# Kernel tuning notes

Hardware: AMD Instinct MI355X
Metric: run time of the kernel (lower is better)

Reference implementation:

```python
import jax, jax.numpy as jnp
import numpy as np

NEG_SLOPE = 0.2

def _gat_conv(x, src, dst, W, a_src, a_dst, b, heads, out_ch, concat):
    N = x.shape[0]
    h = (x @ W).reshape(N, heads, out_ch)                      # [N,H,C]
    al_s = jnp.einsum('nhc,hc->nh', h, a_src)                  # [N,H]
    al_d = jnp.einsum('nhc,hc->nh', h, a_dst)
    e = jax.nn.leaky_relu(al_s[src] + al_d[dst], NEG_SLOPE)    # [E,H]
    emax = jax.ops.segment_max(e, dst, num_segments=N)         # [N,H]
    ex = jnp.exp(e - emax[dst])
    denom = jax.ops.segment_sum(ex, dst, num_segments=N)
    alpha = ex / denom[dst]                                    # [E,H]
    msg = h[src] * alpha[:, :, None]                           # [E,H,C]
    out = jax.ops.segment_sum(msg, dst, num_segments=N)        # [N,H,C]
    if concat:
        out = out.reshape(N, heads * out_ch)
    else:
        out = out.mean(axis=1)
    return out + b

def _add_self_loops(edge_index, N):
    loops = jnp.arange(N, dtype=edge_index.dtype)
    src = jnp.concatenate([edge_index[0], loops])
    dst = jnp.concatenate([edge_index[1], loops])
    return src, dst

def setup_inputs() -> dict:
    key = jax.random.key(0)
    ks = jax.random.split(key, 16)
    N, E, Fin, C, H, G, OUT = 50000, 1600000, 128, 32, 8, 256, 64
    s = 0.05
    inp = {
        'x': jax.random.normal(ks[0], (N, Fin), jnp.float32),
        'edge_index': jax.random.randint(ks[1], (2, E), 0, N, jnp.int64),
        'batch': jnp.sort(jax.random.randint(ks[2], (N,), 0, G, jnp.int64)),
        'W0': jax.random.normal(ks[3], (Fin, H * C), jnp.float32) * s,
        'a_src0': jax.random.normal(ks[4], (H, C), jnp.float32) * s,
        'a_dst0': jax.random.normal(ks[5], (H, C), jnp.float32) * s,
        'b0': jnp.zeros((H * C,), jnp.float32),
        'W1': jax.random.normal(ks[6], (H * C, H * C), jnp.float32) * s,
        'a_src1': jax.random.normal(ks[7], (H, C), jnp.float32) * s,
        'a_dst1': jax.random.normal(ks[8], (H, C), jnp.float32) * s,
        'b1': jnp.zeros((H * C,), jnp.float32),
        'W2': jax.random.normal(ks[9], (H * C, C), jnp.float32) * s,
        'a_src2': jax.random.normal(ks[10], (1, C), jnp.float32) * s,
        'a_dst2': jax.random.normal(ks[11], (1, C), jnp.float32) * s,
        'b2': jnp.zeros((C,), jnp.float32),
        'lin_w': jax.random.normal(ks[12], (C, OUT), jnp.float32) * s,
        'lin_b': jnp.zeros((OUT,), jnp.float32),
    }
    return inp

def reference(x, edge_index, batch, W0, a_src0, a_dst0, b0, W1, a_src1, a_dst1, b1,
              W2, a_src2, a_dst2, b2, lin_w, lin_b):
    N = x.shape[0]
    G = 256
    src, dst = _add_self_loops(edge_index, N)
    h = jax.nn.relu(_gat_conv(x, src, dst, W0, a_src0, a_dst0, b0, 8, 32, True))
    h = jax.nn.relu(_gat_conv(h, src, dst, W1, a_src1, a_dst1, b1, 8, 32, True))
    h = _gat_conv(h, src, dst, W2, a_src2, a_dst2, b2, 1, 32, True)  # heads=1 concat -> [N,32]
    # global mean pool over graphs
    sums = jax.ops.segment_sum(h, batch, num_segments=G)
    cnts = jax.ops.segment_sum(jnp.ones((N,), h.dtype), batch, num_segments=G)
    pooled = sums / jnp.maximum(cnts, 1.0)[:, None]
    return pooled @ lin_w + lin_b
```

## Files before the change

### kernel.cpp

```cpp
#include <hip/hip_runtime.h>
#include <hip/hip_bf16.h>


#define LRELU(x) ((x) >= 0.f ? (x) : 0.2f * (x))

typedef unsigned short ushort8 __attribute__((ext_vector_type(8)));
typedef unsigned short ushort4v __attribute__((ext_vector_type(4)));
typedef __attribute__((ext_vector_type(8))) short bf16x8;
typedef __attribute__((ext_vector_type(4))) float f32x4;

__device__ __forceinline__ float bf2f(unsigned short u) {
    return __uint_as_float(((unsigned)u) << 16);
}
__device__ __forceinline__ unsigned short f2bf(float f) {
    __hip_bfloat16 b = __float2bfloat16(f);
    return *reinterpret_cast<unsigned short*>(&b);
}
__device__ __forceinline__ void gl_lds16(const unsigned short* g, unsigned short* l) {
    __builtin_amdgcn_global_load_lds((const __attribute__((address_space(1))) void*)g,
                                     (__attribute__((address_space(3))) void*)l, 16, 0, 0);
}


__global__ void deg_kernel(const int* __restrict__ dst, int* __restrict__ deg,
                           int E, int N) {
    int i = blockIdx.x * blockDim.x + threadIdx.x;
    if (i < E) atomicAdd(&deg[dst[i]], 1);
    else if (i < E + N) atomicAdd(&deg[i - E], 1);
}

__global__ void scan_kernel(const int* __restrict__ deg, int* __restrict__ rowptr, int n,
                            const int* __restrict__ batch, int* __restrict__ gstart,
                            int N, int G) {
    const int tid = threadIdx.x;
    if (tid <= G) {
        int lo = 0, hi = N;
        while (lo < hi) { int mid = (lo + hi) >> 1; if (batch[mid] < tid) lo = mid + 1; else hi = mid; }
        gstart[tid] = lo;
    }
    __shared__ int partial[1024];
    const int chunk = (n + 1023) / 1024;
    const int start = min(tid * chunk, n);
    const int end = min(start + chunk, n);
    int s = 0;
    for (int i = start; i < end; i++) s += deg[i];
    partial[tid] = s;
    __syncthreads();
    for (int o = 1; o < 1024; o <<= 1) {
        int v = (tid >= o) ? partial[tid - o] : 0;
        __syncthreads();
        partial[tid] += v;
        __syncthreads();
    }
    int run = (tid == 0) ? 0 : partial[tid - 1];
    for (int i = start; i < end; i++) { rowptr[i] = run; run += deg[i]; }
    if (tid == 0) rowptr[n] = partial[1023];
}

__global__ void scatter_col_binned(const int* __restrict__ src, const int* __restrict__ dst,
                                   int* __restrict__ rowptr, int* __restrict__ col,
                                   int E, int N, int lo, int hi) {
    int i = blockIdx.x * blockDim.x + threadIdx.x;
    if (i < E) {
        int d = dst[i];
        if (d < lo || d >= hi) return;
        int pos = atomicAdd(&rowptr[d], 1);
        col[pos] = src[i];
    } else if (i < E + N) {
        int d = i - E;
        if (d < lo || d >= hi) return;
        int pos = atomicAdd(&rowptr[d], 1);
        col[pos] = d;
    }
}


__global__ void prep_kernel(const float* __restrict__ x, const float* __restrict__ W0,
                            const float* __restrict__ W1, const float* __restrict__ W2,
                            unsigned short* __restrict__ xb, unsigned short* __restrict__ w0t,
                            unsigned short* __restrict__ w1t, unsigned short* __restrict__ w2t,
                            int N) {
    int i = blockIdx.x * blockDim.x + threadIdx.x;
    int nx = N * 128;
    if (i < nx) { xb[i] = f2bf(x[i]); return; }
    i -= nx;
    if (i < 256 * 128) {
        int n = i / 128, k = i - n * 128;
        w0t[i] = f2bf(W0[(size_t)k * 256 + n]);
        return;
    }
    i -= 256 * 128;
    if (i < 256 * 256) {
        int n = i / 256, k = i - n * 256;
        w1t[i] = f2bf(W1[(size_t)k * 256 + n]);
        return;
    }
    i -= 256 * 256;
    if (i < 32 * 256) {
        int n = i / 256, k = i - n * 256;
        w2t[i] = f2bf(W2[(size_t)k * 32 + n]);
    }
}


template <int BM, int BN, int WM, int WN, int H>
__global__ __launch_bounds__(256)
void gemm_bf16_al(const unsigned short* __restrict__ A, const unsigned short* __restrict__ Bt,
                  unsigned short* __restrict__ Cc,
                  const float* __restrict__ a_src, const float* __restrict__ a_dst,
                  float* __restrict__ als, float* __restrict__ ald,
                  int M, int Nn, int K) {
    constexpr int BK = 64;
    constexpr int MT = WM / 16, NT = WN / 16;
    constexpr int NWX = BN / WN;
    constexpr int NHL = WN / 32;
    __shared__ __attribute__((aligned(16))) unsigned short Ab[BM][BK];
    __shared__ __attribute__((aligned(16))) unsigned short Bb[BN][BK];
    const int tid = threadIdx.x;
    const int lane = tid & 63;
    const int wave = tid >> 6;
    const int wx = wave % NWX, wy = wave / NWX;
    const int by = blockIdx.y * BM;
    const int bx = blockIdx.x * BN;
    const int r16 = lane & 15, kg = lane >> 4;
    const int srow = lane >> 3, sslot = lane & 7;

    f32x4 acc[MT][NT];
#pragma unroll
    for (int i = 0; i < MT; i++)
#pragma unroll
        for (int j = 0; j < NT; j++) acc[i][j] = (f32x4){0.f, 0.f, 0.f, 0.f};

    for (int k0 = 0; k0 < K; k0 += BK) {
        for (int t = wave; t < BM / 8; t += 4) {
            int gm = by + t * 8 + srow;
            if (gm >= M) gm = M - 1;
            gl_lds16(A + (size_t)gm * K + k0 + sslot * 8, &Ab[t * 8][0]);
        }
        for (int t = wave; t < BN / 8; t += 4) {
            int gn = bx + t * 8 + srow;
            gl_lds16(Bt + (size_t)gn * K + k0 + sslot * 8, &Bb[t * 8][0]);
        }
        __syncthreads();
#pragma unroll
        for (int ks = 0; ks < 2; ks++) {
            bf16x8 bh[NT];
#pragma unroll
            for (int j = 0; j < NT; j++)
                bh[j] = *(const bf16x8*)&Bb[wx * WN + j * 16 + r16][ks * 32 + kg * 8];
#pragma unroll
            for (int i = 0; i < MT; i++) {
                bf16x8 ah = *(const bf16x8*)&Ab[wy * WM + i * 16 + r16][ks * 32 + kg * 8];
#pragma unroll
                for (int j = 0; j < NT; j++)
                    acc[i][j] = __builtin_amdgcn_mfma_f32_16x16x32_bf16(ah, bh[j], acc[i][j], 0, 0, 0);
            }
        }
        __syncthreads();
    }

    const int c0 = bx + wx * WN;
#pragma unroll
    for (int i = 0; i < MT; i++) {
#pragma unroll
        for (int r = 0; r < 4; r++) {
            int gm = by + wy * WM + i * 16 + kg * 4 + r;
            bool ok = gm < M;
            float sa[NHL] = {};
            float sd[NHL] = {};
#pragma unroll
            for (int j = 0; j < NT; j++) {
                int gn = c0 + j * 16 + r16;
                float v = acc[i][j][r];
                if (ok) Cc[(size_t)gm * Nn + gn] = f2bf(v);
                sa[j >> 1] += v * a_src[gn];
                sd[j >> 1] += v * a_dst[gn];
            }
#pragma unroll
            for (int m = 1; m < 16; m <<= 1) {
#pragma unroll
                for (int t = 0; t < NHL; t++) {
                    sa[t] += __shfl_xor(sa[t], m);
                    sd[t] += __shfl_xor(sd[t], m);
                }
            }
            if (ok && r16 == 0) {
#pragma unroll
                for (int t = 0; t < NHL; t++) {
                    int hh = (c0 >> 5) + t;
                    als[(size_t)gm * H + hh] = sa[t];
                    ald[(size_t)gm * H + hh] = sd[t];
                }
            }
        }
    }
}


__global__ __launch_bounds__(256)
void gat_agg_w8(const unsigned short* __restrict__ hfeat,
                const float* __restrict__ als, const float* __restrict__ ald,
                const int* __restrict__ rowptr,
                const int* __restrict__ col,
                const float* __restrict__ bias,
                unsigned short* __restrict__ outH,
                int N) {
    constexpr int CAP = 128;
    const int wid = threadIdx.x >> 6;
    const int lane = threadIdx.x & 63;
    const int n = blockIdx.x * 4 + wid;
    __shared__ float se_all[4][CAP * 8];
    __shared__ int scol_all[4][CAP];
    if (n >= N) return;
    float* se = se_all[wid];
    int* scol = scol_all[wid];

    const int r0 = (n == 0) ? 0 : rowptr[n - 1];
    const int deg = rowptr[n] - r0;
    const int dcap = min(deg, CAP);

    for (int j = lane; j < dcap; j += 64) scol[j] = col[r0 + j];

    const int slot = lane >> 3, h = lane & 7;
    const float aldh = ald[(size_t)n * 8 + h];
    float psum = 0.f;
    for (int j = 0; j < deg; j += 8) {
        int e = j + slot;
        if (e < deg) {
            int s = (e < dcap) ? scol[e] : col[r0 + e];
            float ev = als[(size_t)s * 8 + h] + aldh;
            ev = LRELU(ev);
            float w = __expf(ev);
            psum += w;
            if (e < CAP) se[e * 8 + h] = w;
        }
    }
#pragma unroll
    for (int m = 8; m < 64; m <<= 1) psum += __shfl_xor(psum, m);
    const int q = lane >> 3;
    const float sinv = 1.0f / __shfl(psum, q);
    const float aldq = ald[(size_t)n * 8 + q];

    const int cb = lane * 4;
    float a0 = 0.f, a1 = 0.f, a2 = 0.f, a3 = 0.f;
    int j = 0;
    for (; j + 3 < dcap; j += 4) {
        int s0 = __builtin_amdgcn_readfirstlane(scol[j]);
        int s1 = __builtin_amdgcn_readfirstlane(scol[j + 1]);
        int s2 = __builtin_amdgcn_readfirstlane(scol[j + 2]);
        int s3 = __builtin_amdgcn_readfirstlane(scol[j + 3]);
        ushort4v v0 = *(const ushort4v*)(hfeat + (size_t)s0 * 256 + cb);
        ushort4v v1 = *(const ushort4v*)(hfeat + (size_t)s1 * 256 + cb);
        ushort4v v2 = *(const ushort4v*)(hfeat + (size_t)s2 * 256 + cb);
        ushort4v v3 = *(const ushort4v*)(hfeat + (size_t)s3 * 256 + cb);
        float w0 = se[j * 8 + q];
        float w1 = se[j * 8 + 8 + q];
        float w2 = se[j * 8 + 16 + q];
        float w3 = se[j * 8 + 24 + q];
        a0 += bf2f(v0[0]) * w0; a1 += bf2f(v0[1]) * w0; a2 += bf2f(v0[2]) * w0; a3 += bf2f(v0[3]) * w0;
        a0 += bf2f(v1[0]) * w1; a1 += bf2f(v1[1]) * w1; a2 += bf2f(v1[2]) * w1; a3 += bf2f(v1[3]) * w1;
        a0 += bf2f(v2[0]) * w2; a1 += bf2f(v2[1]) * w2; a2 += bf2f(v2[2]) * w2; a3 += bf2f(v2[3]) * w2;
        a0 += bf2f(v3[0]) * w3; a1 += bf2f(v3[1]) * w3; a2 += bf2f(v3[2]) * w3; a3 += bf2f(v3[3]) * w3;
    }
    for (; j < dcap; j++) {
        int s0 = __builtin_amdgcn_readfirstlane(scol[j]);
        ushort4v v0 = *(const ushort4v*)(hfeat + (size_t)s0 * 256 + cb);
        float w0 = se[j * 8 + q];
        a0 += bf2f(v0[0]) * w0; a1 += bf2f(v0[1]) * w0; a2 += bf2f(v0[2]) * w0; a3 += bf2f(v0[3]) * w0;
    }
    for (; j < deg; j++) {
        int s0 = col[r0 + j];
        float ev = als[(size_t)s0 * 8 + q] + aldq;
        ev = LRELU(ev);
        float w0 = __expf(ev);
        ushort4v v0 = *(const ushort4v*)(hfeat + (size_t)s0 * 256 + cb);
        a0 += bf2f(v0[0]) * w0; a1 += bf2f(v0[1]) * w0; a2 += bf2f(v0[2]) * w0; a3 += bf2f(v0[3]) * w0;
    }

    float4 b4 = *(const float4*)&bias[cb];
    float o0 = fmaxf(a0 * sinv + b4.x, 0.f);
    float o1 = fmaxf(a1 * sinv + b4.y, 0.f);
    float o2 = fmaxf(a2 * sinv + b4.z, 0.f);
    float o3 = fmaxf(a3 * sinv + b4.w, 0.f);
    const size_t ob = (size_t)n * 256 + cb;
    *(ushort4v*)&outH[ob] = (ushort4v){f2bf(o0), f2bf(o1), f2bf(o2), f2bf(o3)};
}


__global__ __launch_bounds__(256)
void gat_agg_h1w(const unsigned short* __restrict__ hfeat,
                 const float* __restrict__ als, const float* __restrict__ ald,
                 const int* __restrict__ rowptr, const int* __restrict__ col,
                 const float* __restrict__ bias, float* __restrict__ out, int N) {
    constexpr int CAP = 256;
    const int wid = threadIdx.x >> 6;
    const int lane = threadIdx.x & 63;
    const int n = blockIdx.x * 4 + wid;
    __shared__ float sw_all[4][CAP];
    __shared__ int scol_all[4][CAP];
    if (n >= N) return;
    float* sw = sw_all[wid];
    int* scol = scol_all[wid];

    const int r0 = (n == 0) ? 0 : rowptr[n - 1];
    const int deg = rowptr[n] - r0;
    const int dcap = min(deg, CAP);
    const float aldn = ald[n];

    float lsum = 0.f;
    for (int idx = lane; idx < deg; idx += 64) {
        int s = col[r0 + idx];
        float ev = als[s] + aldn;
        ev = LRELU(ev);
        float w = __expf(ev);
        if (idx < CAP) { sw[idx] = w; scol[idx] = s; }
        lsum += w;
    }
#pragma unroll
    for (int m = 1; m < 64; m <<= 1) lsum += __shfl_xor(lsum, m);
    const float sinv = 1.0f / lsum;

    const int slot = lane >> 3, ch = lane & 7;
    float a0 = 0.f, a1 = 0.f, a2 = 0.f, a3 = 0.f;
    for (int j = 0; j < dcap; j += 8) {
        int e = j + slot;
        int ec = min(e, dcap - 1);
        int s = scol[ec];
        float w = (e < dcap) ? sw[ec] : 0.f;
        ushort4v v = *(const ushort4v*)(hfeat + (size_t)s * 32 + ch * 4);
        a0 += bf2f(v[0]) * w; a1 += bf2f(v[1]) * w;
        a2 += bf2f(v[2]) * w; a3 += bf2f(v[3]) * w;
    }
    for (int j = CAP; j < deg; j += 8) {
        int e = j + slot;
        int ec = min(e, deg - 1);
        int s = col[r0 + ec];
        float w = 0.f;
        if (e < deg) {
            float ev = als[s] + aldn;
            ev = LRELU(ev);
            w = __expf(ev);
        }
        ushort4v v = *(const ushort4v*)(hfeat + (size_t)s * 32 + ch * 4);
        a0 += bf2f(v[0]) * w; a1 += bf2f(v[1]) * w;
        a2 += bf2f(v[2]) * w; a3 += bf2f(v[3]) * w;
    }
#pragma unroll
    for (int m = 8; m < 64; m <<= 1) {
        a0 += __shfl_xor(a0, m);
        a1 += __shfl_xor(a1, m);
        a2 += __shfl_xor(a2, m);
        a3 += __shfl_xor(a3, m);
    }
    if (slot == 0) {
        float4 b4 = *(const float4*)&bias[ch * 4];
        float4 o;
        o.x = a0 * sinv + b4.x;
        o.y = a1 * sinv + b4.y;
        o.z = a2 * sinv + b4.z;
        o.w = a3 * sinv + b4.w;
        *(float4*)&out[(size_t)n * 32 + ch * 4] = o;
    }
}


__global__ __launch_bounds__(256)
void pool_final_kernel(const float* __restrict__ h, const int* __restrict__ gstart,
                       const float* __restrict__ lin_w, const float* __restrict__ lin_b,
                       float* __restrict__ out) {
    const int g = blockIdx.x;
    const int tid = threadIdx.x;
    const int n0 = gstart[g], n1 = gstart[g + 1];
    const int r = tid >> 5, c = tid & 31;
    __shared__ float pp[4][32];
    __shared__ float pm[32];
    float acc = 0.f;
    for (int n = n0 + r; n < n1; n += 8) acc += h[(size_t)n * 32 + c];
    acc += __shfl_xor(acc, 32);
    if ((tid & 63) < 32) pp[tid >> 6][c] = acc;
    __syncthreads();
    if (tid < 32) {
        float s = pp[0][tid] + pp[1][tid] + pp[2][tid] + pp[3][tid];
        pm[tid] = s / fmaxf((float)(n1 - n0), 1.f);
    }
    __syncthreads();
    if (tid < 64) {
        float a = lin_b[tid];
#pragma unroll 8
        for (int cc = 0; cc < 32; cc++) a += pm[cc] * lin_w[cc * 64 + tid];
        out[(size_t)g * 64 + tid] = a;
    }
}


extern "C" void kernel_launch(void* const* d_in, const int* in_sizes, int n_in,
                              void* d_out, int out_size, void* d_ws, size_t ws_size,
                              hipStream_t stream) {
    const float* x     = (const float*)d_in[0];
    const int*   ei    = (const int*)d_in[1];
    const int*   batch = (const int*)d_in[2];
    const float* W0    = (const float*)d_in[3];
    const float* a_s0  = (const float*)d_in[4];
    const float* a_d0  = (const float*)d_in[5];
    const float* b0    = (const float*)d_in[6];
    const float* W1    = (const float*)d_in[7];
    const float* a_s1  = (const float*)d_in[8];
    const float* a_d1  = (const float*)d_in[9];
    const float* b1    = (const float*)d_in[10];
    const float* W2    = (const float*)d_in[11];
    const float* a_s2  = (const float*)d_in[12];
    const float* a_d2  = (const float*)d_in[13];
    const float* b2    = (const float*)d_in[14];
    const float* lin_w = (const float*)d_in[15];
    const float* lin_b = (const float*)d_in[16];

    const int N = in_sizes[0] / 128;
    const int E = in_sizes[1] / 2;
    const int G = 256;
    const int Etot = E + N;
    const int* src = ei;
    const int* dst = ei + E;

    char* w = (char*)d_ws;
    size_t off = 0;
    auto alloc = [&](size_t bytes) -> void* {
        void* p = (void*)(w + off);
        off += (bytes + 255) & ~(size_t)255;
        return p;
    };
    int* deg    = (int*)alloc((size_t)N * 4);
    int* rowptr = (int*)alloc((size_t)(N + 1) * 4);
    int* colA   = (int*)alloc((size_t)Etot * 4);
    int* gstart = (int*)alloc((size_t)(G + 1) * 4);
    float* als  = (float*)alloc((size_t)N * 8 * 4);
    float* ald  = (float*)alloc((size_t)N * 8 * 4);
    unsigned short* hb  = (unsigned short*)alloc((size_t)N * 256 * 2);
    unsigned short* g0  = (unsigned short*)alloc((size_t)N * 256 * 2);
    float* out2 = (float*)alloc((size_t)N * 32 * 4);
    unsigned short* w0t = (unsigned short*)alloc((size_t)256 * 128 * 2);
    unsigned short* w1t = (unsigned short*)alloc((size_t)256 * 256 * 2);
    unsigned short* w2t = (unsigned short*)alloc((size_t)32 * 256 * 2);
    unsigned short* xb = g0;

    hipMemsetAsync(deg, 0, (size_t)N * 4, stream);

    deg_kernel<<<(Etot + 255) / 256, 256, 0, stream>>>(dst, deg, E, N);
    scan_kernel<<<1, 1024, 0, stream>>>(deg, rowptr, N, batch, gstart, N, G);
    for (int p = 0; p < 2; p++) {
        int lo = (int)((size_t)N * p / 2);
        int hi = (int)((size_t)N * (p + 1) / 2);
        scatter_col_binned<<<(Etot + 255) / 256, 256, 0, stream>>>(src, dst, rowptr, colA, E, N, lo, hi);
    }

    {
        long long tot = (long long)N * 128 + 256 * 128 + 256 * 256 + 32 * 256;
        prep_kernel<<<(int)((tot + 255) / 256), 256, 0, stream>>>(x, W0, W1, W2, xb, w0t, w1t, w2t, N);
    }

    const int MB = (N + 127) / 128;

    gemm_bf16_al<128, 128, 64, 64, 8><<<dim3(2, MB), 256, 0, stream>>>(
        xb, w0t, hb, a_s0, a_d0, als, ald, N, 256, 128);
    gat_agg_w8<<<(N + 3) / 4, 256, 0, stream>>>(hb, als, ald, rowptr, colA, b0, g0, N);

    gemm_bf16_al<128, 128, 64, 64, 8><<<dim3(2, MB), 256, 0, stream>>>(
        g0, w1t, hb, a_s1, a_d1, als, ald, N, 256, 256);
    gat_agg_w8<<<(N + 3) / 4, 256, 0, stream>>>(hb, als, ald, rowptr, colA, b1, g0, N);

    gemm_bf16_al<128, 32, 32, 32, 1><<<dim3(1, MB), 256, 0, stream>>>(
        g0, w2t, hb, a_s2, a_d2, als, ald, N, 32, 256);
    gat_agg_h1w<<<(N + 3) / 4, 256, 0, stream>>>(hb, als, ald, rowptr, colA, b2, out2, N);

    pool_final_kernel<<<G, 256, 0, stream>>>(out2, gstart, lin_w, lin_b, (float*)d_out);
}
```

Measured before the change: 612.8 us.

## Fuse degree count with prep, and CSR scatter with layer-0 GEMM

Measured after the change: 581.4 us (median of 2 runs). 1.05x faster.

```diff
diff --git a/kernel.cpp b/kernel.cpp
--- a/kernel.cpp
+++ b/kernel.cpp
@@ -22,12 +22,134 @@
 }
 
 
-__global__ void deg_kernel(const int* __restrict__ dst, int* __restrict__ deg,
-                           int E, int N) {
-    int i = blockIdx.x * blockDim.x + threadIdx.x;
-    if (i < E) atomicAdd(&deg[dst[i]], 1);
-    else if (i < E + N) atomicAdd(&deg[i - E], 1);
-}
+template <int BM, int BN, int WM, int WN, int H>
+__device__ __forceinline__
+void gemm_core(unsigned short* __restrict__ Ab, unsigned short* __restrict__ Bb,
+               const unsigned short* __restrict__ A, const unsigned short* __restrict__ Bt,
+               unsigned short* __restrict__ Cc,
+               const float* __restrict__ a_src, const float* __restrict__ a_dst,
+               float* __restrict__ als, float* __restrict__ ald,
+               int M, int Nn, int K, int bxi, int byi) {
+    constexpr int BK = 64;
+    constexpr int MT = WM / 16, NT = WN / 16;
+    constexpr int NWX = BN / WN;
+    constexpr int NHL = WN / 32;
+    const int tid = threadIdx.x;
+    const int lane = tid & 63;
+    const int wave = tid >> 6;
+    const int wx = wave % NWX, wy = wave / NWX;
+    const int by = byi * BM;
+    const int bx = bxi * BN;
+    const int r16 = lane & 15, kg = lane >> 4;
+    const int srow = lane >> 3, sslot = lane & 7;
+
+    f32x4 acc[MT][NT];
+#pragma unroll
+    for (int i = 0; i < MT; i++)
+#pragma unroll
+        for (int j = 0; j < NT; j++) acc[i][j] = (f32x4){0.f, 0.f, 0.f, 0.f};
+
+    for (int k0 = 0; k0 < K; k0 += BK) {
+        for (int t = wave; t < BM / 8; t += 4) {
+            int gm = by + t * 8 + srow;
+            if (gm >= M) gm = M - 1;
+            gl_lds16(A + (size_t)gm * K + k0 + sslot * 8, Ab + (t * 8) * BK);
+        }
+        for (int t = wave; t < BN / 8; t += 4) {
+            int gn = bx + t * 8 + srow;
+            gl_lds16(Bt + (size_t)gn * K + k0 + sslot * 8, Bb + (t * 8) * BK);
+        }
+        __syncthreads();
+#pragma unroll
+        for (int ks = 0; ks < 2; ks++) {
+            bf16x8 bh[NT];
+#pragma unroll
+            for (int j = 0; j < NT; j++)
+                bh[j] = *(const bf16x8*)(Bb + (wx * WN + j * 16 + r16) * BK + ks * 32 + kg * 8);
+#pragma unroll
+            for (int i = 0; i < MT; i++) {
+                bf16x8 ah = *(const bf16x8*)(Ab + (wy * WM + i * 16 + r16) * BK + ks * 32 + kg * 8);
+#pragma unroll
+                for (int j = 0; j < NT; j++)
+                    acc[i][j] = __builtin_amdgcn_mfma_f32_16x16x32_bf16(ah, bh[j], acc[i][j], 0, 0, 0);
+            }
+        }
+        __syncthreads();
+    }
+
+    const int c0 = bx + wx * WN;
+#pragma unroll
+    for (int i = 0; i < MT; i++) {
+#pragma unroll
+        for (int r = 0; r < 4; r++) {
+            int gm = by + wy * WM + i * 16 + kg * 4 + r;
+            bool ok = gm < M;
+            float sa[NHL] = {};
+            float sd[NHL] = {};
+#pragma unroll
+            for (int j = 0; j < NT; j++) {
+                int gn = c0 + j * 16 + r16;
+                float v = acc[i][j][r];
+                if (ok) Cc[(size_t)gm * Nn + gn] = f2bf(v);
+                sa[j >> 1] += v * a_src[gn];
+                sd[j >> 1] += v * a_dst[gn];
+            }
+#pragma unroll
+            for (int m = 1; m < 16; m <<= 1) {
+#pragma unroll
+                for (int t = 0; t < NHL; t++) {
+                    sa[t] += __shfl_xor(sa[t], m);
+                    sd[t] += __shfl_xor(sd[t], m);
+                }
+            }
+            if (ok && r16 == 0) {
+#pragma unroll
+                for (int t = 0; t < NHL; t++) {
+                    int hh = (c0 >> 5) + t;
+                    als[(size_t)gm * H + hh] = sa[t];
+                    ald[(size_t)gm * H + hh] = sd[t];
+                }
+            }
+        }
+    }
+}
+
+
+__global__ __launch_bounds__(256)
+void deg_prep_kernel(const int* __restrict__ dst, int* __restrict__ deg, int E, int N,
+                     const float* __restrict__ x, const float* __restrict__ W0,
+                     const float* __restrict__ W1, const float* __restrict__ W2,
+                     unsigned short* __restrict__ xb, unsigned short* __restrict__ w0t,
+                     unsigned short* __restrict__ w1t, unsigned short* __restrict__ w2t,
+                     int DEG_BLKS) {
+    if ((int)blockIdx.x < DEG_BLKS) {
+        int i = blockIdx.x * 256 + threadIdx.x;
+        if (i < E) atomicAdd(&deg[dst[i]], 1);
+        else if (i < E + N) atomicAdd(&deg[i - E], 1);
+        return;
+    }
+    int i = (blockIdx.x - DEG_BLKS) * 256 + threadIdx.x;
+    int nx = N * 128;
+    if (i < nx) { xb[i] = f2bf(x[i]); return; }
+    i -= nx;
+    if (i < 256 * 128) {
+        int n = i / 128, k = i - n * 128;
+        w0t[i] = f2bf(W0[(size_t)k * 256 + n]);
+        return;
+    }
+    i -= 256 * 128;
+    if (i < 256 * 256) {
+        int n = i / 256, k = i - n * 256;
+        w1t[i] = f2bf(W1[(size_t)k * 256 + n]);
+        return;
+    }
+    i -= 256 * 256;
+    if (i < 32 * 256) {
+        int n = i / 256, k = i - n * 256;
+        w2t[i] = f2bf(W2[(size_t)k * 32 + n]);
+    }
+}
+
 
 __global__ void scan_kernel(const int* __restrict__ deg, int* __restrict__ rowptr, int n,
                             const int* __restrict__ batch, int* __restrict__ gstart,
@@ -57,49 +179,35 @@
     if (tid == 0) rowptr[n] = partial[1023];
 }
 
-__global__ void scatter_col_binned(const int* __restrict__ src, const int* __restrict__ dst,
-                                   int* __restrict__ rowptr, int* __restrict__ col,
-                                   int E, int N, int lo, int hi) {
-    int i = blockIdx.x * blockDim.x + threadIdx.x;
-    if (i < E) {
-        int d = dst[i];
-        if (d < lo || d >= hi) return;
-        int pos = atomicAdd(&rowptr[d], 1);
-        col[pos] = src[i];
-    } else if (i < E + N) {
-        int d = i - E;
-        if (d < lo || d >= hi) return;
-        int pos = atomicAdd(&rowptr[d], 1);
-        col[pos] = d;
-    }
-}
-
-
-__global__ void prep_kernel(const float* __restrict__ x, const float* __restrict__ W0,
-                            const float* __restrict__ W1, const float* __restrict__ W2,
-                            unsigned short* __restrict__ xb, unsigned short* __restrict__ w0t,
-                            unsigned short* __restrict__ w1t, unsigned short* __restrict__ w2t,
-                            int N) {
-    int i = blockIdx.x * blockDim.x + threadIdx.x;
-    int nx = N * 128;
-    if (i < nx) { xb[i] = f2bf(x[i]); return; }
-    i -= nx;
-    if (i < 256 * 128) {
-        int n = i / 128, k = i - n * 128;
-        w0t[i] = f2bf(W0[(size_t)k * 256 + n]);
+
+__global__ __launch_bounds__(256)
+void mega0_kernel(const unsigned short* __restrict__ A, const unsigned short* __restrict__ Bt,
+                  unsigned short* __restrict__ Cc,
+                  const float* __restrict__ a_src, const float* __restrict__ a_dst,
+                  float* __restrict__ als, float* __restrict__ ald, int M, int K,
+                  const int* __restrict__ src, const int* __restrict__ dst,
+                  int* __restrict__ rowptr, int* __restrict__ col, int E, int N,
+                  int GEMM_BLKS, int SCAT_BLKS) {
+    __shared__ __attribute__((aligned(16))) unsigned short Ab[128 * 64];
+    __shared__ __attribute__((aligned(16))) unsigned short Bb[128 * 64];
+    const int bid = blockIdx.x;
+    if (bid < GEMM_BLKS) {
+        gemm_core<128, 128, 64, 64, 8>(Ab, Bb, A, Bt, Cc, a_src, a_dst, als, ald,
+                                       M, 256, K, bid & 1, bid >> 1);
         return;
     }
-    i -= 256 * 128;
-    if (i < 256 * 256) {
-        int n = i / 256, k = i - n * 256;
-        w1t[i] = f2bf(W1[(size_t)k * 256 + n]);
-        return;
-    }
-    i -= 256 * 256;
-    if (i < 32 * 256) {
-        int n = i / 256, k = i - n * 256;
-        w2t[i] = f2bf(W2[(size_t)k * 32 + n]);
-    }
+    const int sb = bid - GEMM_BLKS;
+    const int bin = sb / SCAT_BLKS;
+    const int i = (sb - bin * SCAT_BLKS) * 256 + threadIdx.x;
+    const int lo = (int)((long long)N * bin / 4);
+    const int hi = (int)((long long)N * (bin + 1) / 4);
+    int s, d;
+    if (i < E) { d = dst[i]; s = src[i]; }
+    else if (i < E + N) { d = i - E; s = d; }
+    else return;
+    if (d < lo || d >= hi) return;
+    int pos = atomicAdd(&rowptr[d], 1);
+    col[pos] = s;
 }
 
 
@@ -110,90 +218,10 @@
                   const float* __restrict__ a_src, const float* __restrict__ a_dst,
                   float* __restrict__ als, float* __restrict__ ald,
                   int M, int Nn, int K) {
-    constexpr int BK = 64;
-    constexpr int MT = WM / 16, NT = WN / 16;
-    constexpr int NWX = BN / WN;
-    constexpr int NHL = WN / 32;
-    __shared__ __attribute__((aligned(16))) unsigned short Ab[BM][BK];
-    __shared__ __attribute__((aligned(16))) unsigned short Bb[BN][BK];
-    const int tid = threadIdx.x;
-    const int lane = tid & 63;
-    const int wave = tid >> 6;
-    const int wx = wave % NWX, wy = wave / NWX;
-    const int by = blockIdx.y * BM;
-    const int bx = blockIdx.x * BN;
-    const int r16 = lane & 15, kg = lane >> 4;
-    const int srow = lane >> 3, sslot = lane & 7;
-
-    f32x4 acc[MT][NT];
-#pragma unroll
-    for (int i = 0; i < MT; i++)
-#pragma unroll
-        for (int j = 0; j < NT; j++) acc[i][j] = (f32x4){0.f, 0.f, 0.f, 0.f};
-
-    for (int k0 = 0; k0 < K; k0 += BK) {
-        for (int t = wave; t < BM / 8; t += 4) {
-            int gm = by + t * 8 + srow;
-            if (gm >= M) gm = M - 1;
-            gl_lds16(A + (size_t)gm * K + k0 + sslot * 8, &Ab[t * 8][0]);
-        }
-        for (int t = wave; t < BN / 8; t += 4) {
-            int gn = bx + t * 8 + srow;
-            gl_lds16(Bt + (size_t)gn * K + k0 + sslot * 8, &Bb[t * 8][0]);
-        }
-        __syncthreads();
-#pragma unroll
-        for (int ks = 0; ks < 2; ks++) {
-            bf16x8 bh[NT];
-#pragma unroll
-            for (int j = 0; j < NT; j++)
-                bh[j] = *(const bf16x8*)&Bb[wx * WN + j * 16 + r16][ks * 32 + kg * 8];
-#pragma unroll
-            for (int i = 0; i < MT; i++) {
-                bf16x8 ah = *(const bf16x8*)&Ab[wy * WM + i * 16 + r16][ks * 32 + kg * 8];
-#pragma unroll
-                for (int j = 0; j < NT; j++)
-                    acc[i][j] = __builtin_amdgcn_mfma_f32_16x16x32_bf16(ah, bh[j], acc[i][j], 0, 0, 0);
-            }
-        }
-        __syncthreads();
-    }
-
-    const int c0 = bx + wx * WN;
-#pragma unroll
-    for (int i = 0; i < MT; i++) {
-#pragma unroll
-        for (int r = 0; r < 4; r++) {
-            int gm = by + wy * WM + i * 16 + kg * 4 + r;
-            bool ok = gm < M;
-            float sa[NHL] = {};
-            float sd[NHL] = {};
-#pragma unroll
-            for (int j = 0; j < NT; j++) {
-                int gn = c0 + j * 16 + r16;
-                float v = acc[i][j][r];
-                if (ok) Cc[(size_t)gm * Nn + gn] = f2bf(v);
-                sa[j >> 1] += v * a_src[gn];
-                sd[j >> 1] += v * a_dst[gn];
-            }
-#pragma unroll
-            for (int m = 1; m < 16; m <<= 1) {
-#pragma unroll
-                for (int t = 0; t < NHL; t++) {
-                    sa[t] += __shfl_xor(sa[t], m);
-                    sd[t] += __shfl_xor(sd[t], m);
-                }
-            }
-            if (ok && r16 == 0) {
-#pragma unroll
-                for (int t = 0; t < NHL; t++) {
-                    int hh = (c0 >> 5) + t;
-                    als[(size_t)gm * H + hh] = sa[t];
-                    ald[(size_t)gm * H + hh] = sd[t];
-                }
-            }
-        }
-    }
+    __shared__ __attribute__((aligned(16))) unsigned short Ab[BM * 64];
+    __shared__ __attribute__((aligned(16))) unsigned short Bb[BN * 64];
+    gemm_core<BM, BN, WM, WN, H>(Ab, Bb, A, Bt, Cc, a_src, a_dst, als, ald,
+                                 M, Nn, K, blockIdx.x, blockIdx.y);
 }
 
 
@@ -444,23 +472,25 @@
 
     hipMemsetAsync(deg, 0, (size_t)N * 4, stream);
 
-    deg_kernel<<<(Etot + 255) / 256, 256, 0, stream>>>(dst, deg, E, N);
+    {
+        const int DEG_BLKS = (Etot + 255) / 256;
+        long long prep_elems = (long long)N * 128 + 256 * 128 + 256 * 256 + 32 * 256;
+        const int PREP_BLKS = (int)((prep_elems + 255) / 256);
+        deg_prep_kernel<<<DEG_BLKS + PREP_BLKS, 256, 0, stream>>>(
+            dst, deg, E, N, x, W0, W1, W2, xb, w0t, w1t, w2t, DEG_BLKS);
+    }
+
     scan_kernel<<<1, 1024, 0, stream>>>(deg, rowptr, N, batch, gstart, N, G);
-    for (int p = 0; p < 2; p++) {
-        int lo = (int)((size_t)N * p / 2);
-        int hi = (int)((size_t)N * (p + 1) / 2);
-        scatter_col_binned<<<(Etot + 255) / 256, 256, 0, stream>>>(src, dst, rowptr, colA, E, N, lo, hi);
-    }
+
+    const int MB = (N + 127) / 128;
 
     {
-        long long tot = (long long)N * 128 + 256 * 128 + 256 * 256 + 32 * 256;
-        prep_kernel<<<(int)((tot + 255) / 256), 256, 0, stream>>>(x, W0, W1, W2, xb, w0t, w1t, w2t, N);
-    }
-
-    const int MB = (N + 127) / 128;
-
-    gemm_bf16_al<128, 128, 64, 64, 8><<<dim3(2, MB), 256, 0, stream>>>(
-        xb, w0t, hb, a_s0, a_d0, als, ald, N, 256, 128);
+        const int GEMM_BLKS = 2 * MB;
+        const int SCAT_BLKS = (Etot + 255) / 256;
+        mega0_kernel<<<GEMM_BLKS + 4 * SCAT_BLKS, 256, 0, stream>>>(
+            xb, w0t, hb, a_s0, a_d0, als, ald, N, 128,
+            src, dst, rowptr, colA, E, N, GEMM_BLKS, SCAT_BLKS);
+    }
     gat_agg_w8<<<(N + 3) / 4, 256, 0, stream>>>(hb, als, ald, rowptr, colA, b0, g0, N);
 
     gemm_bf16_al<128, 128, 64, 64, 8><<<dim3(2, MB), 256, 0, stream>>>(
```
